# Performance work log

Measured on AMD Instinct MI355X. Metric: run time of the kernel, lower is better.

The kernel has to match this reference:

```python
import jax, jax.numpy as jnp
import numpy as np

N_ATOMS = 512
N_FEATURES = 64
BATCH = 8
BINS = 64
SEG_LEN = 1
LEAKY_SLOPE = 0.01


def _segments(n, length=1):
    # all pairs of segments (i,i+length),(j,j+length), i<j, excluding end1==start2
    n_seg = n - length
    i, j = np.triu_indices(n_seg, k=1)
    seg = np.stack([i, i + length, j, j + length], axis=1)
    return seg[seg[:, 1] != seg[:, 2]].astype(np.int32)


def _nnorm(v):
    return v / jnp.linalg.norm(v, axis=-1, keepdims=True)


def _writhe(segments, xyz):
    # segments: (P,4) int, xyz: (B,N,3) -> (B,P)
    smat = xyz[:, segments]                                  # (B,P,4,3)
    B, P = smat.shape[0], smat.shape[1]
    # displacements r02,r03,r12,r13 (point a in seg1 -> point b in seg2)
    disp = _nnorm((smat[:, :, None, 2:, :] - smat[:, :, :2, None, :]).reshape(B, P, 4, 3))
    idx_a = jnp.array([0, 1, 3, 2])
    idx_b = jnp.array([1, 3, 2, 0])
    crosses = _nnorm(jnp.cross(disp[:, :, idx_a], disp[:, :, idx_b]))
    dots = jnp.clip(jnp.sum(crosses * crosses[:, :, idx_b], axis=-1), -1.0, 1.0)
    omega = jnp.arcsin(dots).sum(-1)                         # (B,P)
    signs = jnp.sign(jnp.sum(
        jnp.cross(_nnorm(smat[:, :, 3] - smat[:, :, 2]), _nnorm(smat[:, :, 1] - smat[:, :, 0]))
        * disp[:, :, 0], axis=-1))
    return omega * signs / (2.0 * jnp.pi)


def _rbf(x, start=-1.0, end=1.0, number=BINS):
    # soft_one_hot_linspace, basis='gaussian', cutoff=False
    values = jnp.linspace(start, end, number, dtype=x.dtype)
    step = values[1] - values[0]
    diff = (x[..., None] - values) / step
    return jnp.exp(-(diff ** 2)) / 1.12


def setup_inputs() -> dict:
    key = jax.random.key(0)
    k = jax.random.split(key, 4)
    seg = jnp.asarray(_segments(N_ATOMS, SEG_LEN))           # (129795,4)
    return {
        "x": jax.random.normal(k[0], (BATCH, N_ATOMS, N_FEATURES), jnp.float32),
        "xyz": jax.random.normal(k[1], (BATCH, N_ATOMS, 3), jnp.float32) * 3.0,
        "segments": seg,
        "W1": jax.random.normal(k[2], (BINS, N_FEATURES), jnp.float32) / np.sqrt(BINS),
        "b1": jnp.zeros((N_FEATURES,), jnp.float32),
        "W2": jax.random.normal(k[3], (N_FEATURES, N_FEATURES), jnp.float32) / np.sqrt(N_FEATURES),
        "b2": jnp.zeros((N_FEATURES,), jnp.float32),
    }


def reference(x, xyz, segments, W1, b1, W2, b2):
    wr = _writhe(segments, xyz)                              # (B,P)
    # bidirectional edges between segment start points
    src = jnp.concatenate([segments[:, 0], segments[:, 2]])  # (E,)
    dst = jnp.concatenate([segments[:, 2], segments[:, 0]])  # (E,)
    wr_e = jnp.concatenate([wr, wr], axis=1)                 # (B,E)
    h = jax.nn.leaky_relu(_rbf(wr_e) @ W1 + b1, LEAKY_SLOPE) # (B,E,F)
    msg = (h @ W2 + b2) * x[:, src]                          # (B,E,F)
    agg = jax.vmap(lambda m: jax.ops.segment_sum(m, dst, num_segments=N_ATOMS))(msg)
    return x + agg                                           # residual update (B,N,F)
```

## Files before the change

kernel.cpp:

```cpp
#include <hip/hip_runtime.h>
#include <hip/hip_bf16.h>
#include <math.h>
#include <stdint.h>

#define N_ATOMS 512
#define NF 64
#define NB 8
#define NBINS 64
#define NSEG 511
#define NTF 8192
#define NSENT 2554
#define ETILES2 254

__device__ __forceinline__ float dot3(float ax, float ay, float az,
                                      float bx, float by, float bz) {
    return fmaf(ax, bx, fmaf(ay, by, az * bz));
}

__device__ __forceinline__ uint16_t bf16_bits(float f) {
    union { __hip_bfloat16 h; uint16_t u; } cv;
    cv.h = __float2bfloat16(f);
    return cv.u;
}

__device__ __forceinline__ float compute_wr(const float* pb, int i, int j) {
    float p0x = pb[3*i+0], p0y = pb[3*i+1], p0z = pb[3*i+2];
    float p1x = pb[3*i+3], p1y = pb[3*i+4], p1z = pb[3*i+5];
    float p2x = pb[3*j+0], p2y = pb[3*j+1], p2z = pb[3*j+2];
    float p3x = pb[3*j+3], p3y = pb[3*j+4], p3z = pb[3*j+5];

    float d0x = p2x-p0x, d0y = p2y-p0y, d0z = p2z-p0z;
    float d1x = p3x-p0x, d1y = p3y-p0y, d1z = p3z-p0z;
    float d2x = p2x-p1x, d2y = p2y-p1y, d2z = p2z-p1z;
    float d3x = p3x-p1x, d3y = p3y-p1y, d3z = p3z-p1z;
    {
        float n0 = rsqrtf(dot3(d0x,d0y,d0z,d0x,d0y,d0z)); d0x*=n0; d0y*=n0; d0z*=n0;
        float n1 = rsqrtf(dot3(d1x,d1y,d1z,d1x,d1y,d1z)); d1x*=n1; d1y*=n1; d1z*=n1;
        float n2 = rsqrtf(dot3(d2x,d2y,d2z,d2x,d2y,d2z)); d2x*=n2; d2y*=n2; d2z*=n2;
        float n3 = rsqrtf(dot3(d3x,d3y,d3z,d3x,d3y,d3z)); d3x*=n3; d3y*=n3; d3z*=n3;
    }
    float c0x = d0y*d1z - d0z*d1y, c0y = d0z*d1x - d0x*d1z, c0z = d0x*d1y - d0y*d1x;
    float c1x = d1y*d3z - d1z*d3y, c1y = d1z*d3x - d1x*d3z, c1z = d1x*d3y - d1y*d3x;
    float c3x = d2y*d0z - d2z*d0y, c3y = d2z*d0x - d2x*d0z, c3z = d2x*d0y - d2y*d0x;
    {
        float n0 = rsqrtf(dot3(c0x,c0y,c0z,c0x,c0y,c0z)); c0x*=n0; c0y*=n0; c0z*=n0;
        float n1 = rsqrtf(dot3(c1x,c1y,c1z,c1x,c1y,c1z)); c1x*=n1; c1y*=n1; c1z*=n1;
        float n3 = rsqrtf(dot3(c3x,c3y,c3z,c3x,c3y,c3z)); c3x*=n3; c3y*=n3; c3z*=n3;
    }
    float t0 = fminf(fmaxf(dot3(c0x,c0y,c0z, c1x,c1y,c1z), -1.f), 1.f);
    float t1 = fminf(fmaxf(dot3(c1x,c1y,c1z, c3x,c3y,c3z), -1.f), 1.f);
    float t3 = fminf(fmaxf(dot3(c3x,c3y,c3z, c0x,c0y,c0z), -1.f), 1.f);
    float omega = asinf(t0) + asinf(t1) + asinf(t3) + 1.5707963267948966f;
    float ex = p3x-p2x, ey = p3y-p2y, ez = p3z-p2z;
    float fx = p1x-p0x, fy = p1y-p0y, fz = p1z-p0z;
    float gx = ey*fz - ez*fy, gy = ez*fx - ex*fz, gz = ex*fy - ey*fx;
    float sgd = dot3(gx,gy,gz, d0x,d0y,d0z);
    float sgn = (sgd > 0.f) ? 1.f : ((sgd < 0.f) ? -1.f : 0.f);
    return omega * sgn * 0.15915494309189535f;
}

__device__ __forceinline__ uint32_t wr_to_off(float w) {
    float tf = (w + 1.0f) * ((float)(NTF - 1) * 0.5f);
    tf = fminf(fmaxf(tf, 0.0f), (float)(NTF - 1));
    int t0 = (int)(tf + 0.5f);
    t0 = (t0 > NTF - 1) ? (NTF - 1) : t0;
    return (uint32_t)t0 << 6;
}

__launch_bounds__(256)
__global__ void prepass(
        const float* __restrict__ xyz, const int* __restrict__ seg,
        const float* __restrict__ W1, const float* __restrict__ b1,
        const float* __restrict__ W2, const float* __restrict__ b2,
        uint16_t* __restrict__ tabh, uint32_t* __restrict__ ta, int P) {
    __shared__ float lds[1536];

    const unsigned bx = blockIdx.x;

    if (bx < NTF / 8) {
        const int widx = threadIdx.x >> 6;
        const int lane = threadIdx.x & 63;
        const int g = bx * 4 + widx;
        const int g2 = g + NTF / 2;

        float tta = ((-1.0f + (2.0f / (float)(NTF - 1)) * (float)g)  + 1.0f) * 31.5f;
        float ttb = ((-1.0f + (2.0f / (float)(NTF - 1)) * (float)g2) + 1.0f) * 31.5f;

        float a0=0.f,a1=0.f,a2=0.f,a3=0.f, e0=0.f,e1=0.f,e2=0.f,e3=0.f;
        #pragma unroll
        for (int k = 0; k < NBINS; k += 4) {
            #pragma unroll
            for (int q = 0; q < 4; ++q) {
                float da = tta - (float)(k + q);
                float db = ttb - (float)(k + q);
                float ra = __expf(-da * da) * 0.8928571428571429f;
                float rb = __expf(-db * db) * 0.8928571428571429f;
                float wv = W1[(k + q) * NF + lane];
                if (q == 0) { a0 = fmaf(ra, wv, a0); e0 = fmaf(rb, wv, e0); }
                if (q == 1) { a1 = fmaf(ra, wv, a1); e1 = fmaf(rb, wv, e1); }
                if (q == 2) { a2 = fmaf(ra, wv, a2); e2 = fmaf(rb, wv, e2); }
                if (q == 3) { a3 = fmaf(ra, wv, a3); e3 = fmaf(rb, wv, e3); }
            }
        }
        float ha = ((a0 + a1) + (a2 + a3)) + b1[lane];
        float hb = ((e0 + e1) + (e2 + e3)) + b1[lane];
        ha = fmaxf(ha, 0.01f * ha);
        hb = fmaxf(hb, 0.01f * hb);
        lds[widx * 64 + lane]       = ha;
        lds[256 + widx * 64 + lane] = hb;
        __syncthreads();

        float m0=0.f,m1=0.f,m2=0.f,m3=0.f, n0=0.f,n1=0.f,n2=0.f,n3=0.f;
        #pragma unroll
        for (int k = 0; k < NF; k += 4) {
            float w0 = W2[(k + 0) * NF + lane];
            float w1v = W2[(k + 1) * NF + lane];
            float w2v = W2[(k + 2) * NF + lane];
            float w3 = W2[(k + 3) * NF + lane];
            m0 = fmaf(lds[widx * 64 + k + 0], w0, m0);
            m1 = fmaf(lds[widx * 64 + k + 1], w1v, m1);
            m2 = fmaf(lds[widx * 64 + k + 2], w2v, m2);
            m3 = fmaf(lds[widx * 64 + k + 3], w3, m3);
            n0 = fmaf(lds[256 + widx * 64 + k + 0], w0, n0);
            n1 = fmaf(lds[256 + widx * 64 + k + 1], w1v, n1);
            n2 = fmaf(lds[256 + widx * 64 + k + 2], w2v, n2);
            n3 = fmaf(lds[256 + widx * 64 + k + 3], w3, n3);
        }
        float ma = ((m0 + m1) + (m2 + m3)) + b2[lane];
        float mb = ((n0 + n1) + (n2 + n3)) + b2[lane];
        tabh[g  * NF + lane] = bf16_bits(ma);
        tabh[g2 * NF + lane] = bf16_bits(mb);
        if (g == 0) tabh[NTF * NF + lane] = 0;
    } else if (bx < NTF / 8 + NB * ETILES2) {
        const int rel = bx - NTF / 8;
        const int b = rel / ETILES2;
        const int tile = rel - b * ETILES2;

        const float* xb = xyz + b * (N_ATOMS * 3);
        #pragma unroll
        for (int k = 0; k < 6; ++k)
            lds[k * 256 + threadIdx.x] = xb[k * 256 + threadIdx.x];
        __syncthreads();

        #pragma unroll
        for (int q = 0; q < 2; ++q) {
            const int e = tile * 512 + q * 256 + threadIdx.x;
            if (e < P) {
                int4 sv = ((const int4*)seg)[e];
                const int i = sv.x;
                const int j = sv.z;
                uint32_t u = wr_to_off(compute_wr(lds, i, j));
                ta[(b << 18) + (i << 9) + j] = u;
                ta[(b << 18) + (j << 9) + i] = u;
            }
        }
    } else {
        const int idx = (bx - (NTF / 8 + NB * ETILES2)) * 256 + threadIdx.x;
        if (idx < NB * NSENT) {
            const int b = idx / NSENT;
            const int k = idx - b * NSENT;
            int d, s;
            if      (k < 512)  { d = k;        s = k;     }
            else if (k < 1023) { d = k - 512;  s = d + 1; }
            else if (k < 1534) { s = k - 1023; d = s + 1; }
            else if (k < 2044) { d = k - 1534; s = NSEG;  }
            else               { s = k - 2044; d = NSEG;  }
            ta[(b << 18) + (d << 9) + s] = (uint32_t)NTF << 6;
        }
    }
}

__launch_bounds__(1024, 8)
__global__ void agg16(
        const float* __restrict__ x, const uint32_t* __restrict__ ta,
        const uint16_t* __restrict__ tabh, float* __restrict__ out) {
    __shared__ float xs[16384];

    const int tid  = threadIdx.x;
    const int widx = tid >> 6;
    const int lane = tid & 63;
    const int fl   = lane & 15;
    const int rw   = lane >> 4;
    const int h    = widx >> 3;
    const int r    = widx & 7;
    const int ht   = tid & 511;
    const int bid  = blockIdx.x;
    const int b    = bid >> 6;
    const int dst  = ((bid & 63) << 3) + r;

    const float* xb = x + ((size_t)b << 15);
    const uint32_t* tarow = ta + ((size_t)b << 18) + ((size_t)dst << 9);

    {
        const float* xsrc = xb + ((h * 4) << 12);
        float* xdst = xs + (h << 12);
        #pragma unroll
        for (int k = 0; k < 8; ++k)
            xdst[k * 512 + ht] = xsrc[k * 512 + ht];
    }

    const bool c1 = (lane & 16) != 0;
    const bool c2 = (lane & 32) != 0;
    const int  feidx = fl << 2;

    float acc0 = 0.f, acc1 = 0.f, acc2 = 0.f, acc3 = 0.f;
    #pragma unroll
    for (int p = 0; p < 4; ++p) {
        const int c = h * 4 + p;
        const int tavc = (int)tarow[(c << 6) + lane];

        __syncthreads();

        if (p < 3) {
            const float* xsrc = xb + ((c + 1) << 12);
            float* xdst = xs + ((((p + 1) & 1) << 13) + (h << 12));
            #pragma unroll
            for (int k = 0; k < 8; ++k)
                xdst[k * 512 + ht] = xsrc[k * 512 + ht];
        }

        const float* xc = xs + (((p & 1) << 13) + (h << 12));
        #pragma unroll
        for (int g4 = 0; g4 < 16; g4 += 4) {
            uint2 mw[4];
            #pragma unroll
            for (int q = 0; q < 4; ++q) {
                const int g = g4 + q;
                const uint32_t o0 =
                    (uint32_t)__builtin_amdgcn_readlane(tavc, 4 * g + 0);
                const uint32_t o1 =
                    (uint32_t)__builtin_amdgcn_readlane(tavc, 4 * g + 1);
                const uint32_t o2 =
                    (uint32_t)__builtin_amdgcn_readlane(tavc, 4 * g + 2);
                const uint32_t o3 =
                    (uint32_t)__builtin_amdgcn_readlane(tavc, 4 * g + 3);
                const uint32_t oA = c1 ? o1 : o0;
                const uint32_t oB = c1 ? o3 : o2;
                const uint32_t osel = c2 ? oB : oA;
                mw[q] = *(const uint2*)(tabh + osel + feidx);
            }
            #pragma unroll
            for (int q = 0; q < 4; ++q) {
                const int g = g4 + q;
                const float4 xv =
                    *(const float4*)(xc + (g << 8) + (rw << 6) + feidx);
                const float m0 = __uint_as_float(mw[q].x << 16);
                const float m1 = __uint_as_float(mw[q].x & 0xffff0000u);
                const float m2 = __uint_as_float(mw[q].y << 16);
                const float m3 = __uint_as_float(mw[q].y & 0xffff0000u);
                acc0 = fmaf(m0, xv.x, acc0);
                acc1 = fmaf(m1, xv.y, acc1);
                acc2 = fmaf(m2, xv.z, acc2);
                acc3 = fmaf(m3, xv.w, acc3);
            }
        }
    }
    acc0 += __shfl_xor(acc0, 16); acc0 += __shfl_xor(acc0, 32);
    acc1 += __shfl_xor(acc1, 16); acc1 += __shfl_xor(acc1, 32);
    acc2 += __shfl_xor(acc2, 16); acc2 += __shfl_xor(acc2, 32);
    acc3 += __shfl_xor(acc3, 16); acc3 += __shfl_xor(acc3, 32);

    __syncthreads();
    if (h == 1 && rw == 0) {
        float4 v; v.x = acc0; v.y = acc1; v.z = acc2; v.w = acc3;
        *(float4*)&xs[(r << 6) + feidx] = v;
    }
    __syncthreads();
    if (h == 0 && rw == 0) {
        const float4 prev = *(const float4*)&xs[(r << 6) + feidx];
        const float4 xv   = *(const float4*)(xb + (dst << 6) + feidx);
        float4 res;
        res.x = xv.x + acc0 + prev.x;
        res.y = xv.y + acc1 + prev.y;
        res.z = xv.z + acc2 + prev.z;
        res.w = xv.w + acc3 + prev.w;
        *(float4*)(out + ((size_t)b << 15) + (dst << 6) + feidx) = res;
    }
}


__global__ void init_out_kernel(const float* __restrict__ x, float* __restrict__ out, int n) {
    int idx = blockIdx.x * blockDim.x + threadIdx.x;
    if (idx < n) out[idx] = x[idx];
}

__device__ __forceinline__ void compute_m(
        const float* __restrict__ pb, int i, int j,
        const float* __restrict__ W1, const float* __restrict__ b1,
        const float* __restrict__ W2, const float* __restrict__ b2,
        float* __restrict__ mout) {
    float wr = compute_wr(pb, i, j);
    float acc_[NBINS];
    {
        float tt = (wr + 1.0f) * 31.5f;
        #pragma unroll
        for (int k = 0; k < NBINS; ++k) {
            float d = tt - (float)k;
            acc_[k] = __expf(-d * d) * 0.8928571428571429f;
        }
    }
    float h_[NF];
    #pragma unroll
    for (int f = 0; f < NF; ++f) h_[f] = b1[f];
    #pragma unroll
    for (int k = 0; k < NBINS; ++k) {
        float r = acc_[k];
        #pragma unroll
        for (int f = 0; f < NF; ++f) h_[f] = fmaf(r, W1[k * NF + f], h_[f]);
    }
    #pragma unroll
    for (int f = 0; f < NF; ++f) h_[f] = fmaxf(h_[f], 0.01f * h_[f]);
    #pragma unroll
    for (int f = 0; f < NF; ++f) acc_[f] = b2[f];
    #pragma unroll
    for (int k = 0; k < NF; ++k) {
        float hk = h_[k];
        #pragma unroll
        for (int f = 0; f < NF; ++f) acc_[f] = fmaf(hk, W2[k * NF + f], acc_[f]);
    }
    #pragma unroll
    for (int f = 0; f < NF; ++f) mout[f] = acc_[f];
}

__launch_bounds__(256, 2)
__global__ void writhe_msg_atomic_kernel(
        const float* __restrict__ x, const float* __restrict__ xyz,
        const int* __restrict__ seg,
        const float* __restrict__ W1, const float* __restrict__ b1,
        const float* __restrict__ W2, const float* __restrict__ b2,
        float* __restrict__ out, int P, int n_tiles) {
    __shared__ __hip_bfloat16 lds_m[4][64 * 65];
    __shared__ int lds_i[4][64];
    __shared__ int lds_j[4][64];

    const int widx = threadIdx.x >> 6;
    const int lane = threadIdx.x & 63;
    const int wave_g = blockIdx.x * 4 + widx;
    const int b = wave_g / n_tiles;
    const int tile = wave_g - b * n_tiles;
    const int bc = (b < NB) ? b : 0;
    const int e = tile * 64 + lane;
    const bool valid = (b < NB) && (e < P);

    int4 sv = valid ? ((const int4*)seg)[e] : make_int4(0, 1, 2, 3);
    const int i = sv.x;
    const int j = sv.z;

    float m[NF];
    compute_m(xyz + bc * (N_ATOMS * 3), i, j, W1, b1, W2, b2, m);

    const float scale = valid ? 1.0f : 0.0f;
    #pragma unroll
    for (int f = 0; f < NF; ++f)
        lds_m[widx][lane * 65 + f] = __float2bfloat16(m[f] * scale);
    lds_i[widx][lane] = i;
    lds_j[widx][lane] = j;
    __syncthreads();

    const float* xb = x + bc * (N_ATOMS * NF);
    float* ob = out + bc * (N_ATOMS * NF);
    int cur_i = lds_i[widx][0];
    float acc_i = 0.0f;
    for (int ee = 0; ee < 64; ++ee) {
        int ie = lds_i[widx][ee];
        int je = lds_j[widx][ee];
        float mv = __bfloat162float(lds_m[widx][ee * 65 + lane]);
        float xi = xb[ie * NF + lane];
        float xj = xb[je * NF + lane];
        atomicAdd(&ob[je * NF + lane], mv * xi);
        if (ie != cur_i) {
            atomicAdd(&ob[cur_i * NF + lane], acc_i);
            acc_i = 0.0f;
            cur_i = ie;
        }
        acc_i = fmaf(mv, xj, acc_i);
    }
    atomicAdd(&ob[cur_i * NF + lane], acc_i);
}

extern "C" void kernel_launch(void* const* d_in, const int* in_sizes, int n_in,
                              void* d_out, int out_size, void* d_ws, size_t ws_size,
                              hipStream_t stream) {
    const float* x   = (const float*)d_in[0];
    const float* xyz = (const float*)d_in[1];
    const int*   seg = (const int*)d_in[2];
    const float* W1  = (const float*)d_in[3];
    const float* b1  = (const float*)d_in[4];
    const float* W2  = (const float*)d_in[5];
    const float* b2  = (const float*)d_in[6];
    float* out = (float*)d_out;

    const int P = in_sizes[2] / 4;
    const int n_tiles = (P + 63) / 64;

    const size_t tabh_bytes = (size_t)(NTF + 1) * NF * sizeof(uint16_t);
    const size_t ta_bytes   = (size_t)NB * N_ATOMS * N_ATOMS * sizeof(uint32_t);
    const size_t need_ws = tabh_bytes + ta_bytes;

    if (ws_size >= need_ws && P <= ETILES2 * 512) {
        uint16_t* tabh = (uint16_t*)d_ws;
        uint32_t* ta   = (uint32_t*)((char*)d_ws + tabh_bytes);

        const int nsent_blocks = (NB * NSENT + 255) / 256;
        const int total_blocks = NTF / 8 + NB * ETILES2 + nsent_blocks;
        hipLaunchKernelGGL(prepass, dim3(total_blocks), dim3(256), 0, stream,
                           xyz, seg, W1, b1, W2, b2, tabh, ta, P);

        hipLaunchKernelGGL(agg16, dim3(NB * 64), dim3(1024), 0, stream,
                           x, ta, tabh, out);
    } else {
        const int n = out_size;
        hipLaunchKernelGGL(init_out_kernel, dim3((n + 255) / 256), dim3(256), 0, stream,
                           x, out, n);
        const int total_waves = NB * n_tiles;
        const int blocks = (total_waves + 3) / 4;
        hipLaunchKernelGGL(writhe_msg_atomic_kernel, dim3(blocks), dim3(256), 0, stream,
                           x, xyz, seg, W1, b1, W2, b2, out, P, n_tiles);
    }
}
```

Baseline: 109.3 us.

## Read x directly from global memory in aggregation kernel instead of LDS staging

The aggregation kernel no longer stages x chunks through a 64KB double-buffered shared-memory tile with per-chunk barriers. Each thread loads its float4 of x straight from global memory (relying on L1/L2 caching) and prefetches all four table-offset words up front. The readlane-and-select offset picking becomes a single shuffle. This removes the barriers and the LDS footprint, so more blocks can be resident, but x is now read repeatedly from cache instead of once per block.

```diff
diff --git a/kernel.cpp b/kernel.cpp
--- a/kernel.cpp
+++ b/kernel.cpp
@@ -171,10 +171,10 @@
 }
 
 __launch_bounds__(1024, 8)
-__global__ void agg16(
+__global__ void agg17(
         const float* __restrict__ x, const uint32_t* __restrict__ ta,
         const uint16_t* __restrict__ tabh, float* __restrict__ out) {
-    __shared__ float xs[16384];
+    __shared__ float xs[512];
 
     const int tid  = threadIdx.x;
     const int widx = tid >> 6;
@@ -183,75 +183,43 @@
     const int rw   = lane >> 4;
     const int h    = widx >> 3;
     const int r    = widx & 7;
-    const int ht   = tid & 511;
     const int bid  = blockIdx.x;
     const int b    = bid >> 6;
     const int dst  = ((bid & 63) << 3) + r;
+    const int feidx = fl << 2;
+
+    const uint32_t* tarow =
+        ta + ((size_t)b << 18) + ((size_t)dst << 9) + (h << 8);
+    const int tv0 = (int)tarow[lane];
+    const int tv1 = (int)tarow[64 + lane];
+    const int tv2 = (int)tarow[128 + lane];
+    const int tv3 = (int)tarow[192 + lane];
 
     const float* xb = x + ((size_t)b << 15);
-    const uint32_t* tarow = ta + ((size_t)b << 18) + ((size_t)dst << 9);
-
-    {
-        const float* xsrc = xb + ((h * 4) << 12);
-        float* xdst = xs + (h << 12);
-        #pragma unroll
-        for (int k = 0; k < 8; ++k)
-            xdst[k * 512 + ht] = xsrc[k * 512 + ht];
-    }
-
-    const bool c1 = (lane & 16) != 0;
-    const bool c2 = (lane & 32) != 0;
-    const int  feidx = fl << 2;
+    const float* xh = xb + (h << 14) + (rw << 6) + feidx;
 
     float acc0 = 0.f, acc1 = 0.f, acc2 = 0.f, acc3 = 0.f;
     #pragma unroll
-    for (int p = 0; p < 4; ++p) {
-        const int c = h * 4 + p;
-        const int tavc = (int)tarow[(c << 6) + lane];
-
-        __syncthreads();
-
-        if (p < 3) {
-            const float* xsrc = xb + ((c + 1) << 12);
-            float* xdst = xs + ((((p + 1) & 1) << 13) + (h << 12));
-            #pragma unroll
-            for (int k = 0; k < 8; ++k)
-                xdst[k * 512 + ht] = xsrc[k * 512 + ht];
-        }
-
-        const float* xc = xs + (((p & 1) << 13) + (h << 12));
+    for (int cc = 0; cc < 4; ++cc) {
+        const int tvc = (cc == 0) ? tv0 : (cc == 1) ? tv1 : (cc == 2) ? tv2 : tv3;
+        const float* xc = xh + (cc << 12);
         #pragma unroll
         for (int g4 = 0; g4 < 16; g4 += 4) {
-            uint2 mw[4];
+            uint2  mw[4];
+            float4 xv[4];
             #pragma unroll
             for (int q = 0; q < 4; ++q) {
-                const int g = g4 + q;
-                const uint32_t o0 =
-                    (uint32_t)__builtin_amdgcn_readlane(tavc, 4 * g + 0);
-                const uint32_t o1 =
-                    (uint32_t)__builtin_amdgcn_readlane(tavc, 4 * g + 1);
-                const uint32_t o2 =
-                    (uint32_t)__builtin_amdgcn_readlane(tavc, 4 * g + 2);
-                const uint32_t o3 =
-                    (uint32_t)__builtin_amdgcn_readlane(tavc, 4 * g + 3);
-                const uint32_t oA = c1 ? o1 : o0;
-                const uint32_t oB = c1 ? o3 : o2;
-                const uint32_t osel = c2 ? oB : oA;
+                const int gg = g4 + q;
+                const int osel = __shfl(tvc, 4 * gg + rw);
                 mw[q] = *(const uint2*)(tabh + osel + feidx);
+                xv[q] = *(const float4*)(xc + (gg << 8));
             }
             #pragma unroll
             for (int q = 0; q < 4; ++q) {
-                const int g = g4 + q;
-                const float4 xv =
-                    *(const float4*)(xc + (g << 8) + (rw << 6) + feidx);
-                const float m0 = __uint_as_float(mw[q].x << 16);
-                const float m1 = __uint_as_float(mw[q].x & 0xffff0000u);
-                const float m2 = __uint_as_float(mw[q].y << 16);
-                const float m3 = __uint_as_float(mw[q].y & 0xffff0000u);
-                acc0 = fmaf(m0, xv.x, acc0);
-                acc1 = fmaf(m1, xv.y, acc1);
-                acc2 = fmaf(m2, xv.z, acc2);
-                acc3 = fmaf(m3, xv.w, acc3);
+                acc0 = fmaf(__uint_as_float(mw[q].x << 16),          xv[q].x, acc0);
+                acc1 = fmaf(__uint_as_float(mw[q].x & 0xffff0000u),  xv[q].y, acc1);
+                acc2 = fmaf(__uint_as_float(mw[q].y << 16),          xv[q].z, acc2);
+                acc3 = fmaf(__uint_as_float(mw[q].y & 0xffff0000u),  xv[q].w, acc3);
             }
         }
     }
@@ -260,7 +228,6 @@
     acc2 += __shfl_xor(acc2, 16); acc2 += __shfl_xor(acc2, 32);
     acc3 += __shfl_xor(acc3, 16); acc3 += __shfl_xor(acc3, 32);
 
-    __syncthreads();
     if (h == 1 && rw == 0) {
         float4 v; v.x = acc0; v.y = acc1; v.z = acc2; v.w = acc3;
         *(float4*)&xs[(r << 6) + feidx] = v;
@@ -406,7 +373,7 @@
         hipLaunchKernelGGL(prepass, dim3(total_blocks), dim3(256), 0, stream,
                            xyz, seg, W1, b1, W2, b2, tabh, ta, P);
 
-        hipLaunchKernelGGL(agg16, dim3(NB * 64), dim3(1024), 0, stream,
+        hipLaunchKernelGGL(agg17, dim3(NB * 64), dim3(1024), 0, stream,
                            x, ta, tabh, out);
     } else {
         const int n = out_size;
```

Measured after the change: 118.5 us. 8.4% more time.
